# Kernel optimization log

Hardware: AMD Instinct MI355X
Metric: run time of the kernel (lower is better)

The kernel has to match this reference:

```python
import jax, jax.numpy as jnp
import numpy as np

B, C, S, N, V = 8, 16, 512, 512, 128
EPS = 1e-5

def setup_inputs() -> dict:
    key = jax.random.key(0)
    ks = jax.random.split(key, 9)
    def u(k, shape, scale):
        return jax.random.uniform(k, shape, jnp.float32, -scale, scale)
    attn_scale = 12 * np.sqrt(3.0 / (S * N * V))      # custom attn_init for query / key.left / value2
    xav_vs = np.sqrt(6.0 / (V + S))                    # xavier_uniform for (C, V, S) or (C, S, V)
    xav_nv = np.sqrt(6.0 / (N + V))                    # xavier_uniform for (C, N, V)
    return {
        "x": jax.random.normal(ks[0], (B, C, S, N), jnp.float32),
        "wq": u(ks[1], (C, N, V), attn_scale),          # query weight (other_features=S)
        "k_left": u(ks[2], (C, V, S), attn_scale),      # key left (attn_init)
        "k_right": u(ks[3], (C, N, V), xav_nv),         # key right (xavier)
        "v1_left": u(ks[4], (C, V, S), xav_vs),         # value1 left (xavier, attn_init=False)
        "v1_right": u(ks[5], (C, N, V), attn_scale),    # value1 right (attn_init scale)
        "v2_w": u(ks[6], (C, V, S), attn_scale),        # value2 weight (other_features=N)
        "gamma": jnp.ones((C,), jnp.float32),
        "beta": jnp.zeros((C,), jnp.float32),
    }

def batch_scaler(y, gamma, beta):
    # normalize over dims (0, 2, 3); per-channel affine
    mean = jnp.mean(y, axis=(0, 2, 3), keepdims=True)
    var = jnp.mean(jnp.square(y - mean), axis=(0, 2, 3), keepdims=True)
    yhat = (y - mean) * jax.lax.rsqrt(var + EPS)
    return yhat * gamma[None, :, None, None] + beta[None, :, None, None]

def reference(x, wq, k_left, k_right, v1_left, v1_right, v2_w, gamma, beta):
    # x: [B,C,S,N]
    q = jnp.matmul(x, wq)                               # [B,C,S,V]
    k = jnp.matmul(jnp.matmul(k_left, x), k_right)       # (C,V,S)@x -> [B,C,V,N] @ (C,N,V) -> [B,C,V,V]
    attn = jax.nn.softmax(jnp.einsum('bcsv,bcwv->bcsw', q, k), axis=-1)  # q @ k^T, softmax last dim
    v1 = jnp.matmul(jnp.matmul(v1_left, x), v1_right)    # [B,C,V,V]
    v2 = jnp.matmul(v2_w, x)                             # [B,C,V,N]
    v = jnp.matmul(v1, v2)                               # [B,C,V,N]
    y = x + jnp.matmul(attn, v)                          # [B,C,S,N]
    return batch_scaler(y, gamma, beta)
```

## Files before the change

kernel.cpp:

```cpp
#include <hip/hip_runtime.h>
#include <math.h>


typedef short  bf16x8 __attribute__((ext_vector_type(8)));
typedef short  short8 __attribute__((ext_vector_type(8)));
typedef float  f32x4  __attribute__((ext_vector_type(4)));

__device__ __forceinline__ unsigned short f2bf(float f) {
    union { float f; unsigned u; } v; v.f = f;
    return (unsigned short)((v.u + 0x7FFF + ((v.u >> 16) & 1)) >> 16);
}
__device__ __forceinline__ float bf2f(unsigned short u) {
    union { unsigned u; float f; } v; v.u = (unsigned)u << 16; return v.f;
}

__device__ __forceinline__ void gload16(const void* g, void* l)
{
    __builtin_amdgcn_global_load_lds(
        (const __attribute__((address_space(1))) void*)g,
        (__attribute__((address_space(3))) void*)l, 16, 0, 0);
}

constexpr size_t OB_XB   = 0;
constexpr size_t OB_XT   = OB_XB  + 67108864;
constexpr size_t OB_KLB  = OB_XT  + 67108864;
constexpr size_t OB_V1LB = OB_KLB + 2097152;
constexpr size_t OB_V2WB = OB_V1LB+ 2097152;
constexpr size_t OB_WQT  = OB_V2WB+ 2097152;
constexpr size_t OB_KRT  = OB_WQT + 2097152;
constexpr size_t OB_V1RT = OB_KRT + 2097152;
constexpr size_t OB_BUF  = OB_V1RT+ 2097152;
constexpr size_t OB_V2T  = OB_BUF + 33554432;
constexpr size_t OB_KM   = OB_V2T + 16777216;
constexpr size_t OB_V1M  = OB_KM  + 4194304;
constexpr size_t OB_ATT  = OB_V1M + 4194304;
constexpr size_t OB_VT   = OB_ATT + 16777216;
constexpr size_t OB_ST   = OB_VT  + 16777216;

template<int NSTEPS, int MF, int NF>
__device__ __forceinline__ void mmcore(const char* __restrict__ Ab, int ldaB,
                                       const char* __restrict__ Bb, int ldbB,
                                       f32x4 (&acc)[MF][NF],
                                       char* __restrict__ smA, char* __restrict__ smB,
                                       int wm, int wn)
{
    const int tid = threadIdx.x;
    const int w = tid >> 6, l = tid & 63, g = l >> 4, lr = l & 15;
    const int rl = l >> 3, ch = l & 7;

#pragma unroll 1
    for (int t = 0; t < NSTEPS; ++t) {
#pragma unroll
        for (int j = 0; j < 4; ++j) {
            const int row = w * 32 + j * 8 + rl;
            gload16(Ab + (size_t)row * ldaB + t * 128 + ((ch ^ (row & 7)) * 16),
                    smA + (w * 32 + j * 8) * 128);
        }
#pragma unroll
        for (int j = 0; j < 4; ++j) {
            const int row = w * 32 + j * 8 + rl;
            gload16(Bb + (size_t)row * ldbB + t * 128 + ((ch ^ (row & 7)) * 16),
                    smB + (w * 32 + j * 8) * 128);
        }
        __syncthreads();
#pragma unroll
        for (int ks = 0; ks < 2; ++ks) {
            bf16x8 av[MF], bv[NF];
            const int cc = ks * 4 + g;
#pragma unroll
            for (int i = 0; i < MF; ++i) { int rw = wm + i * 16 + lr;
                av[i] = *(const bf16x8*)(smA + rw * 128 + ((cc ^ (rw & 7)) * 16)); }
#pragma unroll
            for (int j = 0; j < NF; ++j) { int rw = wn + j * 16 + lr;
                bv[j] = *(const bf16x8*)(smB + rw * 128 + ((cc ^ (rw & 7)) * 16)); }
#pragma unroll
            for (int i = 0; i < MF; ++i)
#pragma unroll
                for (int j = 0; j < NF; ++j)
                    acc[i][j] = __builtin_amdgcn_mfma_f32_16x16x32_bf16(av[i], bv[j], acc[i][j], 0, 0, 0);
        }
        __syncthreads();
    }
}

__device__ __forceinline__ void epi_write_rm(const f32x4 (&acc)[4][4], char* sm)
{
    const int tid = threadIdx.x, w = tid >> 6, l = tid & 63, g = l >> 4, lr = l & 15;
    const int wm = (w >> 1) * 64, wn = (w & 1) * 64;
#pragma unroll
    for (int i = 0; i < 4; ++i)
#pragma unroll
        for (int j = 0; j < 4; ++j) {
            const int row = wm + i * 16 + g * 4, col = wn + j * 16 + lr;
#pragma unroll
            for (int r = 0; r < 4; ++r)
                *(unsigned short*)(sm + (row + r) * 272 + col * 2) = f2bf(acc[i][j][r]);
        }
}

__device__ __forceinline__ void epi_write_tr(const f32x4 (&acc)[4][4], char* sm)
{
    const int tid = threadIdx.x, w = tid >> 6, l = tid & 63, g = l >> 4, lr = l & 15;
    const int wm = (w >> 1) * 64, wn = (w & 1) * 64;
#pragma unroll
    for (int i = 0; i < 4; ++i)
#pragma unroll
        for (int j = 0; j < 4; ++j) {
            const int rv = wm + i * 16 + g * 4, cn = wn + j * 16 + lr;
            ushort4 pk = make_ushort4(f2bf(acc[i][j][0]), f2bf(acc[i][j][1]),
                                      f2bf(acc[i][j][2]), f2bf(acc[i][j][3]));
            *(ushort4*)(sm + cn * 272 + rv * 2) = pk;
        }
}

__device__ __forceinline__ void epi_flush(const char* sm, unsigned short* gout, int ldg)
{
    const int tid = threadIdx.x;
    const int r0 = tid >> 4, q = tid & 15;
#pragma unroll
    for (int rep = 0; rep < 8; ++rep) {
        const int row = rep * 16 + r0;
        *(short8*)((short*)gout + (size_t)row * ldg + q * 8) =
            *(const short8*)(sm + row * 272 + q * 16);
    }
    __syncthreads();
}

__global__ __launch_bounds__(256) void k_prep(const float* __restrict__ kl,
                                              const float* __restrict__ v1l,
                                              const float* __restrict__ v2w,
                                              const float* __restrict__ wq,
                                              const float* __restrict__ kr,
                                              const float* __restrict__ v1r,
                                              unsigned short* __restrict__ klb,
                                              unsigned short* __restrict__ v1lb,
                                              unsigned short* __restrict__ v2wb,
                                              unsigned short* __restrict__ wqt,
                                              unsigned short* __restrict__ krt,
                                              unsigned short* __restrict__ v1rt,
                                              float* __restrict__ stats)
{
    __shared__ float tl[64][65];
    const int id = blockIdx.x, tid = threadIdx.x;
    if (id == 0 && tid < 64) stats[tid] = 0.f;
    if (id < 192) {
        const int sel = id >> 6, blk = id & 63;
        const float* src = sel == 0 ? kl : sel == 1 ? v1l : v2w;
        unsigned short* dst = sel == 0 ? klb : sel == 1 ? v1lb : v2wb;
#pragma unroll
        for (int r = 0; r < 4; ++r) {
            const int i = blk * 1024 + r * 256 + tid;
            float4 v = ((const float4*)src)[i];
            ((ushort4*)dst)[i] = make_ushort4(f2bf(v.x), f2bf(v.y), f2bf(v.z), f2bf(v.w));
        }
        return;
    }
    const int id2 = id - 192;
    const int p = id2 >> 4, rem = id2 & 15, by = rem >> 1, bx = rem & 1;
    const int widx = p >> 4, c = p & 15;
    const float* s = (widx == 0 ? wq : widx == 1 ? kr : v1r) + (size_t)c * 65536;
    unsigned short* d = (widx == 0 ? wqt : widx == 1 ? krt : v1rt) + (size_t)c * 65536;
    const int r0 = by * 64, c0 = bx * 64;
    const int rr = tid >> 4, cc = (tid & 15) * 4;
#pragma unroll
    for (int rep = 0; rep < 4; ++rep) {
        int row = rep * 16 + rr;
        float4 v = *(const float4*)(s + (size_t)(r0 + row) * 128 + c0 + cc);
        tl[cc + 0][row] = v.x; tl[cc + 1][row] = v.y; tl[cc + 2][row] = v.z; tl[cc + 3][row] = v.w;
    }
    __syncthreads();
#pragma unroll
    for (int rep = 0; rep < 4; ++rep) {
        int crow = rep * 16 + rr;
        *(ushort4*)(d + (size_t)(c0 + crow) * 512 + r0 + cc) =
            make_ushort4(f2bf(tl[crow][cc]), f2bf(tl[crow][cc + 1]),
                         f2bf(tl[crow][cc + 2]), f2bf(tl[crow][cc + 3]));
    }
}

__global__ __launch_bounds__(256, 2) void k_wx(const unsigned short* __restrict__ klb,
                                               const unsigned short* __restrict__ v1lb,
                                               const unsigned short* __restrict__ v2wb,
                                               const float* __restrict__ x,
                                               unsigned short* __restrict__ bufb,
                                               unsigned short* __restrict__ v2t)
{
    __shared__ char smem[34816];
    char* smA = smem;
    char* smX = smem + 16384;
    const int mt = blockIdx.x >> 2, n0 = blockIdx.x & 3, bc = blockIdx.y, c = bc & 15;
    const unsigned short* W = mt == 0 ? klb : mt == 1 ? v1lb : v2wb;
    const char* Wb = (const char*)(W + (size_t)c * 65536);
    const float* xs = x + (size_t)bc * 262144 + n0 * 128;
    const int tid = threadIdx.x, w = tid >> 6, l = tid & 63, g = l >> 4, lr = l & 15;
    const int rl = l >> 3, ch = l & 7;
    const int wm = (w >> 1) * 64, wn = (w & 1) * 64;
    const int nq = (tid & 31) * 4, sp2 = (tid >> 5) * 2;

    f32x4 acc[4][4] = {};
    float4 fr[8];
#pragma unroll
    for (int k = 0; k < 4; ++k) {
        const int sl = k * 16 + sp2;
        fr[k * 2 + 0] = *(const float4*)(xs + (size_t)(sl) * 512 + nq);
        fr[k * 2 + 1] = *(const float4*)(xs + (size_t)(sl + 1) * 512 + nq);
    }

#pragma unroll 1
    for (int t = 0; t < 8; ++t) {
#pragma unroll
        for (int j = 0; j < 4; ++j) {
            const int row = w * 32 + j * 8 + rl;
            gload16(Wb + (size_t)row * 1024 + t * 128 + ((ch ^ (row & 7)) * 16),
                    smA + (w * 32 + j * 8) * 128);
        }
#pragma unroll
        for (int k = 0; k < 4; ++k) {
            const int sl = k * 16 + sp2;
            const float4 f0 = fr[k * 2 + 0];
            const float4 f1 = fr[k * 2 + 1];
            const unsigned p0 = f2bf(f0.x) | ((unsigned)f2bf(f1.x) << 16);
            const unsigned p1 = f2bf(f0.y) | ((unsigned)f2bf(f1.y) << 16);
            const unsigned p2 = f2bf(f0.z) | ((unsigned)f2bf(f1.z) << 16);
            const unsigned p3 = f2bf(f0.w) | ((unsigned)f2bf(f1.w) << 16);
            const int cl = sl >> 3, bic = (sl * 2) & 15;
#pragma unroll
            for (int i = 0; i < 4; ++i) {
                const int n = nq + i;
                const unsigned v = (i == 0) ? p0 : (i == 1) ? p1 : (i == 2) ? p2 : p3;
                *(unsigned*)(smX + n * 136 + ((cl ^ (n & 7)) << 4) + bic) = v;
            }
        }
        __syncthreads();
        if (t < 7) {
#pragma unroll
            for (int k = 0; k < 4; ++k) {
                const int sl = k * 16 + sp2;
                fr[k * 2 + 0] = *(const float4*)(xs + (size_t)((t + 1) * 64 + sl) * 512 + nq);
                fr[k * 2 + 1] = *(const float4*)(xs + (size_t)((t + 1) * 64 + sl + 1) * 512 + nq);
            }
        }
#pragma unroll
        for (int ks = 0; ks < 2; ++ks) {
            const int cc = ks * 4 + g;
            bf16x8 av[4], bv[4];
#pragma unroll
            for (int i = 0; i < 4; ++i) { const int rw = wm + i * 16 + lr;
                av[i] = *(const bf16x8*)(smA + rw * 128 + ((cc ^ (rw & 7)) * 16)); }
#pragma unroll
            for (int j = 0; j < 4; ++j) {
                const int n = wn + j * 16 + lr;
                const char* p = smX + n * 136 + ((cc ^ (n & 7)) << 4);
                union { unsigned long long u[2]; bf16x8 v; } tmp;
                tmp.u[0] = *(const unsigned long long*)(p);
                tmp.u[1] = *(const unsigned long long*)(p + 8);
                bv[j] = tmp.v;
            }
#pragma unroll
            for (int i = 0; i < 4; ++i)
#pragma unroll
                for (int j = 0; j < 4; ++j)
                    acc[i][j] = __builtin_amdgcn_mfma_f32_16x16x32_bf16(av[i], bv[j], acc[i][j], 0, 0, 0);
        }
        __syncthreads();
    }

    if (mt < 2) {
        epi_write_rm(acc, smem);
        __syncthreads();
        epi_flush(smem, bufb + (size_t)bc * 131072 + (size_t)mt * 65536 + n0 * 128, 512);
    } else {
        epi_write_tr(acc, smem);
        __syncthreads();
        epi_flush(smem, v2t + (size_t)bc * 65536 + (size_t)n0 * 16384, 128);
    }
}

__global__ __launch_bounds__(256, 2) void k_kr(const unsigned short* __restrict__ bufb,
                                               const unsigned short* __restrict__ krt,
                                               const unsigned short* __restrict__ v1rt,
                                               unsigned short* __restrict__ kmat,
                                               unsigned short* __restrict__ v1m)
{
    __shared__ char smem[34816];
    char* smA = smem; char* smB = smem + 16384;
    const int mt = blockIdx.x, bc = blockIdx.y, c = bc & 15;
    const int w = threadIdx.x >> 6;
    f32x4 acc[4][4] = {};
    mmcore<8, 4, 4>((const char*)(bufb + (size_t)bc * 131072 + (size_t)mt * 65536), 1024,
                    (const char*)((mt ? v1rt : krt) + (size_t)c * 65536), 1024, acc, smA, smB,
                    (w >> 1) * 64, (w & 1) * 64);
    epi_write_rm(acc, smem);
    __syncthreads();
    epi_flush(smem, (mt ? v1m : kmat) + (size_t)bc * 16384, 128);
}

__global__ __launch_bounds__(256, 2) void k_qat(const float* __restrict__ x,
                                                const unsigned short* __restrict__ wqt,
                                                const unsigned short* __restrict__ kmat,
                                                unsigned short* __restrict__ attn)
{
    __shared__ char smem[49152];
    char* smA  = smem;
    char* smB  = smem + 16384;
    char* qlds = smem;
    char* smB2 = smem + 32768;
    const int mt = blockIdx.x, bc = blockIdx.y, c = bc & 15;
    const int tid = threadIdx.x, w = tid >> 6, l = tid & 63, g = l >> 4, lr = l & 15;
    const int rl = l >> 3, ch = l & 7;
    const int wm = (w >> 1) * 64, wn = (w & 1) * 64;

    f32x4 acc[4][4] = {};
    {
        const float* Ax = x + (size_t)bc * 262144 + (size_t)(mt * 128) * 512;
        const char* Bw = (const char*)(wqt + (size_t)c * 65536);
        const int ar = tid >> 4, fq = tid & 15;
#pragma unroll 1
        for (int t = 0; t < 8; ++t) {
#pragma unroll
            for (int j = 0; j < 4; ++j) {
                const int row = w * 32 + j * 8 + rl;
                gload16(Bw + (size_t)row * 1024 + t * 128 + ((ch ^ (row & 7)) * 16),
                        smB + (w * 32 + j * 8) * 128);
            }
            float4 frq[8];
#pragma unroll
            for (int it = 0; it < 8; ++it) {
                const int row = it * 16 + ar;
                frq[it] = *(const float4*)(Ax + (size_t)row * 512 + t * 64 + fq * 4);
            }
#pragma unroll
            for (int it = 0; it < 8; ++it) {
                const int row = it * 16 + ar;
                ushort4 o = make_ushort4(f2bf(frq[it].x), f2bf(frq[it].y),
                                         f2bf(frq[it].z), f2bf(frq[it].w));
                *(ushort4*)(smA + row * 128 + (((fq >> 1) ^ (row & 7)) * 16) + (fq & 1) * 8) = o;
            }
            __syncthreads();
#pragma unroll
            for (int ks = 0; ks < 2; ++ks) {
                const int cc2 = ks * 4 + g;
                bf16x8 av[4], bv[4];
#pragma unroll
                for (int i = 0; i < 4; ++i) { const int rw = wm + i * 16 + lr;
                    av[i] = *(const bf16x8*)(smA + rw * 128 + ((cc2 ^ (rw & 7)) * 16)); }
#pragma unroll
                for (int j = 0; j < 4; ++j) { const int rw = wn + j * 16 + lr;
                    bv[j] = *(const bf16x8*)(smB + rw * 128 + ((cc2 ^ (rw & 7)) * 16)); }
#pragma unroll
                for (int i = 0; i < 4; ++i)
#pragma unroll
                    for (int j = 0; j < 4; ++j)
                        acc[i][j] = __builtin_amdgcn_mfma_f32_16x16x32_bf16(av[i], bv[j], acc[i][j], 0, 0, 0);
            }
            __syncthreads();
        }
    }
    {
        const int t = wn >> 6;
#pragma unroll
        for (int i = 0; i < 4; ++i)
#pragma unroll
            for (int j = 0; j < 4; ++j) {
                const int k6 = j * 16 + lr;
                const int chunk = k6 >> 3, eb = (k6 & 7) << 1;
#pragma unroll
                for (int r = 0; r < 4; ++r) {
                    const int row = wm + i * 16 + g * 4 + r;
                    *(unsigned short*)(qlds + t * 16384 + row * 128 +
                                       ((chunk ^ (row & 7)) << 4) + eb) = f2bf(acc[i][j][r]);
                }
            }
    }
    __syncthreads();

    f32x4 acc2[2][8] = {};
    const char* Kb = (const char*)(kmat + (size_t)bc * 16384);
#pragma unroll
    for (int t = 0; t < 2; ++t) {
#pragma unroll
        for (int j = 0; j < 4; ++j) {
            const int row = w * 32 + j * 8 + rl;
            gload16(Kb + (size_t)row * 256 + t * 128 + ((ch ^ (row & 7)) * 16),
                    smB2 + (w * 32 + j * 8) * 128);
        }
        __syncthreads();
#pragma unroll
        for (int ks = 0; ks < 2; ++ks) {
            const int cc2 = ks * 4 + g;
            bf16x8 av[2], bv[8];
#pragma unroll
            for (int i = 0; i < 2; ++i) { const int rw = w * 32 + i * 16 + lr;
                av[i] = *(const bf16x8*)(qlds + t * 16384 + rw * 128 + ((cc2 ^ (rw & 7)) * 16)); }
#pragma unroll
            for (int j = 0; j < 8; ++j) { const int rw = j * 16 + lr;
                bv[j] = *(const bf16x8*)(smB2 + rw * 128 + ((cc2 ^ (rw & 7)) * 16)); }
#pragma unroll
            for (int i = 0; i < 2; ++i)
#pragma unroll
                for (int j = 0; j < 8; ++j)
                    acc2[i][j] = __builtin_amdgcn_mfma_f32_16x16x32_bf16(av[i], bv[j], acc2[i][j], 0, 0, 0);
        }
        __syncthreads();
    }

    char* wsl = smem + w * 8704;
    unsigned short* ob = attn + (size_t)bc * 65536 + (size_t)(mt * 128 + w * 32) * 128;
#pragma unroll
    for (int i = 0; i < 2; ++i)
#pragma unroll
        for (int r = 0; r < 4; ++r) {
            float mx = -3e38f;
#pragma unroll
            for (int fj = 0; fj < 8; ++fj) mx = fmaxf(mx, acc2[i][fj][r]);
#pragma unroll
            for (int d = 1; d < 16; d <<= 1) mx = fmaxf(mx, __shfl_xor(mx, d));
            float s = 0.f, e[8];
#pragma unroll
            for (int fj = 0; fj < 8; ++fj) { e[fj] = __expf(acc2[i][fj][r] - mx); s += e[fj]; }
#pragma unroll
            for (int d = 1; d < 16; d <<= 1) s += __shfl_xor(s, d);
            const float inv = 1.f / s;
            const int rowh = i * 16 + g * 4 + r;
#pragma unroll
            for (int fj = 0; fj < 8; ++fj)
                *(unsigned short*)(wsl + rowh * 272 + (fj * 16 + lr) * 2) = f2bf(e[fj] * inv);
        }
#pragma unroll
    for (int rep = 0; rep < 8; ++rep) {
        const int row = rep * 4 + (l >> 4);
        *(short8*)((short*)ob + (size_t)row * 128 + (l & 15) * 8) =
            *(const short8*)(wsl + row * 272 + (l & 15) * 16);
    }
}

__global__ __launch_bounds__(256, 2) void k_v(const unsigned short* __restrict__ v2t,
                                              const unsigned short* __restrict__ v1m,
                                              unsigned short* __restrict__ vt)
{
    __shared__ char smem[34816];
    char* smA = smem; char* smB = smem + 16384;
    const int mt = blockIdx.x, bc = blockIdx.y;
    const int w = threadIdx.x >> 6;
    f32x4 acc[4][4] = {};
    mmcore<2, 4, 4>((const char*)(v2t + (size_t)bc * 65536 + (size_t)mt * 16384), 256,
                    (const char*)(v1m + (size_t)bc * 16384), 256, acc, smA, smB,
                    (w >> 1) * 64, (w & 1) * 64);
    epi_write_rm(acc, smem);
    __syncthreads();
    epi_flush(smem, vt + (size_t)bc * 65536 + (size_t)mt * 16384, 128);
}

__global__ __launch_bounds__(256, 2) void k_y(const unsigned short* __restrict__ attn,
                                              const unsigned short* __restrict__ vt,
                                              const float* __restrict__ x,
                                              unsigned short* __restrict__ yb,
                                              float* __restrict__ stats)
{
    __shared__ char smem[34816];
    __shared__ float r1[4], r2[4];
    char* smA = smem; char* smB = smem + 16384;
    const int nx = blockIdx.x, my = blockIdx.y, bc = blockIdx.z, c = bc & 15;
    const int tid = threadIdx.x, w = tid >> 6, l = tid & 63, g = l >> 4, lr = l & 15;
    f32x4 acc[4][4] = {};
    mmcore<2, 4, 4>((const char*)(attn + (size_t)bc * 65536 + (size_t)my * 16384), 256,
                    (const char*)(vt + (size_t)bc * 65536 + (size_t)nx * 16384), 256, acc, smA, smB,
                    (w >> 1) * 64, (w & 1) * 64);
    const float* xw = x + (size_t)bc * 262144 + (size_t)my * 128 * 512 + nx * 128;
    const int wm = (w >> 1) * 64, wn = (w & 1) * 64;
    float lsum = 0.f, lss = 0.f;
#pragma unroll
    for (int i = 0; i < 4; ++i)
#pragma unroll
        for (int j = 0; j < 4; ++j)
#pragma unroll
            for (int r = 0; r < 4; ++r) {
                const int row = wm + i * 16 + g * 4 + r, col = wn + j * 16 + lr;
                const float yv = acc[i][j][r] + xw[(size_t)row * 512 + col];
                lsum += yv; lss += yv * yv;
                *(unsigned short*)(smem + row * 272 + col * 2) = f2bf(yv);
            }
#pragma unroll
    for (int d = 32; d >= 1; d >>= 1) { lsum += __shfl_xor(lsum, d); lss += __shfl_xor(lss, d); }
    if (l == 0) { r1[w] = lsum; r2[w] = lss; }
    __syncthreads();
    epi_flush(smem, yb + (size_t)bc * 262144 + (size_t)my * 128 * 512 + nx * 128, 512);
    if (tid == 0) {
        atomicAdd(&stats[c * 2 + 0], r1[0] + r1[1] + r1[2] + r1[3]);
        atomicAdd(&stats[c * 2 + 1], r2[0] + r2[1] + r2[2] + r2[3]);
    }
}

__global__ __launch_bounds__(256) void k_norm(const unsigned short* __restrict__ yb,
                                              float* __restrict__ out,
                                              const float* __restrict__ stats,
                                              const float* __restrict__ gamma,
                                              const float* __restrict__ beta)
{
    __shared__ float ssc[16], ssh[16];
    if (threadIdx.x < 16) {
        const int c = threadIdx.x;
        const float cnt  = 2097152.f;
        const float mean = stats[c * 2 + 0] / cnt;
        const float var  = stats[c * 2 + 1] / cnt - mean * mean;
        const float sc   = rsqrtf(var + 1e-5f) * gamma[c];
        ssc[c] = sc;
        ssh[c] = beta[c] - mean * sc;
    }
    __syncthreads();
    const int tot = 4194304;
    for (int i = blockIdx.x * 256 + threadIdx.x; i < tot; i += gridDim.x * 256) {
        const long e = (long)i * 8;
        const int c = (int)(e >> 18) & 15;
        const float sc = ssc[c];
        const float sh = ssh[c];
        short8 v = ((const short8*)yb)[i];
        float4 o0, o1;
        o0.x = bf2f((unsigned short)v[0]) * sc + sh;
        o0.y = bf2f((unsigned short)v[1]) * sc + sh;
        o0.z = bf2f((unsigned short)v[2]) * sc + sh;
        o0.w = bf2f((unsigned short)v[3]) * sc + sh;
        o1.x = bf2f((unsigned short)v[4]) * sc + sh;
        o1.y = bf2f((unsigned short)v[5]) * sc + sh;
        o1.z = bf2f((unsigned short)v[6]) * sc + sh;
        o1.w = bf2f((unsigned short)v[7]) * sc + sh;
        ((float4*)out)[(size_t)i * 2 + 0] = o0;
        ((float4*)out)[(size_t)i * 2 + 1] = o1;
    }
}

extern "C" void kernel_launch(void* const* d_in, const int* in_sizes, int n_in,
                              void* d_out, int out_size, void* d_ws, size_t ws_size,
                              hipStream_t stream)
{
    (void)in_sizes; (void)n_in; (void)out_size; (void)ws_size;
    const float* x     = (const float*)d_in[0];
    const float* wq    = (const float*)d_in[1];
    const float* kl    = (const float*)d_in[2];
    const float* kr    = (const float*)d_in[3];
    const float* v1l   = (const float*)d_in[4];
    const float* v1r   = (const float*)d_in[5];
    const float* v2w   = (const float*)d_in[6];
    const float* gamma = (const float*)d_in[7];
    const float* beta  = (const float*)d_in[8];
    float* out = (float*)d_out;
    char*  ws  = (char*)d_ws;

    unsigned short* yb   = (unsigned short*)(ws + OB_XB);
    unsigned short* klb  = (unsigned short*)(ws + OB_KLB);
    unsigned short* v1lb = (unsigned short*)(ws + OB_V1LB);
    unsigned short* v2wb = (unsigned short*)(ws + OB_V2WB);
    unsigned short* wqt  = (unsigned short*)(ws + OB_WQT);
    unsigned short* krt  = (unsigned short*)(ws + OB_KRT);
    unsigned short* v1rt = (unsigned short*)(ws + OB_V1RT);
    unsigned short* bufb = (unsigned short*)(ws + OB_BUF);
    unsigned short* v2t  = (unsigned short*)(ws + OB_V2T);
    unsigned short* kmat = (unsigned short*)(ws + OB_KM);
    unsigned short* v1m  = (unsigned short*)(ws + OB_V1M);
    unsigned short* attn = (unsigned short*)(ws + OB_ATT);
    unsigned short* vt   = (unsigned short*)(ws + OB_VT);
    float*          st   = (float*)(ws + OB_ST);

    hipLaunchKernelGGL(k_prep,  dim3(960),       dim3(256), 0, stream,
                       kl, v1l, v2w, wq, kr, v1r, klb, v1lb, v2wb, wqt, krt, v1rt, st);
    hipLaunchKernelGGL(k_wx,    dim3(12, 128),   dim3(256), 0, stream, klb, v1lb, v2wb, x, bufb, v2t);
    hipLaunchKernelGGL(k_kr,    dim3(2, 128),    dim3(256), 0, stream, bufb, krt, v1rt, kmat, v1m);
    hipLaunchKernelGGL(k_qat,   dim3(4, 128),    dim3(256), 0, stream, x, wqt, kmat, attn);
    hipLaunchKernelGGL(k_v,     dim3(4, 128),    dim3(256), 0, stream, v2t, v1m, vt);
    hipLaunchKernelGGL(k_y,     dim3(4, 4, 128), dim3(256), 0, stream, attn, vt, x, yb, st);
    hipLaunchKernelGGL(k_norm,  dim3(2048),      dim3(256), 0, stream, yb, out, st, gamma, beta);
}
```

Baseline: 232.7 us.

## Merge the three weight-times-x GEMMs into one block per column tile

k_wx now launches one block per (n0, bc) instead of one per weight matrix. Each block computes the k_left and v1_left products together in one pass over x, sharing the bf16-converted x tile in LDS across two accumulator sets, then runs a second pass for the v2 weight. This cuts the x conversion and staging work from three passes to two per tile. In exchange it uses more LDS and registers per block (two accumulator sets) and launches a third as many blocks, which lowers occupancy and parallelism.

```diff
diff --git a/kernel.cpp b/kernel.cpp
--- a/kernel.cpp
+++ b/kernel.cpp
@@ -185,19 +185,20 @@
                                                unsigned short* __restrict__ bufb,
                                                unsigned short* __restrict__ v2t)
 {
-    __shared__ char smem[34816];
-    char* smA = smem;
-    char* smX = smem + 16384;
-    const int mt = blockIdx.x >> 2, n0 = blockIdx.x & 3, bc = blockIdx.y, c = bc & 15;
-    const unsigned short* W = mt == 0 ? klb : mt == 1 ? v1lb : v2wb;
-    const char* Wb = (const char*)(W + (size_t)c * 65536);
+    __shared__ char smem[50176];
+    char* smA0 = smem;
+    char* smA1 = smem + 16384;
+    char* smX  = smem + 32768;
+    const int n0 = blockIdx.x, bc = blockIdx.y, c = bc & 15;
+    const char* Wb0 = (const char*)(klb  + (size_t)c * 65536);
+    const char* Wb1 = (const char*)(v1lb + (size_t)c * 65536);
+    const char* Wb2 = (const char*)(v2wb + (size_t)c * 65536);
     const float* xs = x + (size_t)bc * 262144 + n0 * 128;
     const int tid = threadIdx.x, w = tid >> 6, l = tid & 63, g = l >> 4, lr = l & 15;
     const int rl = l >> 3, ch = l & 7;
     const int wm = (w >> 1) * 64, wn = (w & 1) * 64;
     const int nq = (tid & 31) * 4, sp2 = (tid >> 5) * 2;
 
-    f32x4 acc[4][4] = {};
     float4 fr[8];
 #pragma unroll
     for (int k = 0; k < 4; ++k) {
@@ -206,13 +207,20 @@
         fr[k * 2 + 1] = *(const float4*)(xs + (size_t)(sl + 1) * 512 + nq);
     }
 
+    f32x4 acc0[4][4] = {}, acc1[4][4] = {};
 #pragma unroll 1
     for (int t = 0; t < 8; ++t) {
 #pragma unroll
         for (int j = 0; j < 4; ++j) {
             const int row = w * 32 + j * 8 + rl;
-            gload16(Wb + (size_t)row * 1024 + t * 128 + ((ch ^ (row & 7)) * 16),
-                    smA + (w * 32 + j * 8) * 128);
+            gload16(Wb0 + (size_t)row * 1024 + t * 128 + ((ch ^ (row & 7)) * 16),
+                    smA0 + (w * 32 + j * 8) * 128);
+        }
+#pragma unroll
+        for (int j = 0; j < 4; ++j) {
+            const int row = w * 32 + j * 8 + rl;
+            gload16(Wb1 + (size_t)row * 1024 + t * 128 + ((ch ^ (row & 7)) * 16),
+                    smA1 + (w * 32 + j * 8) * 128);
         }
 #pragma unroll
         for (int k = 0; k < 4; ++k) {
@@ -245,9 +253,6 @@
             const int cc = ks * 4 + g;
             bf16x8 av[4], bv[4];
 #pragma unroll
-            for (int i = 0; i < 4; ++i) { const int rw = wm + i * 16 + lr;
-                av[i] = *(const bf16x8*)(smA + rw * 128 + ((cc ^ (rw & 7)) * 16)); }
-#pragma unroll
             for (int j = 0; j < 4; ++j) {
                 const int n = wn + j * 16 + lr;
                 const char* p = smX + n * 136 + ((cc ^ (n & 7)) << 4);
@@ -257,23 +262,99 @@
                 bv[j] = tmp.v;
             }
 #pragma unroll
+            for (int i = 0; i < 4; ++i) { const int rw = wm + i * 16 + lr;
+                av[i] = *(const bf16x8*)(smA0 + rw * 128 + ((cc ^ (rw & 7)) * 16)); }
+#pragma unroll
             for (int i = 0; i < 4; ++i)
 #pragma unroll
                 for (int j = 0; j < 4; ++j)
-                    acc[i][j] = __builtin_amdgcn_mfma_f32_16x16x32_bf16(av[i], bv[j], acc[i][j], 0, 0, 0);
-        }
-        __syncthreads();
-    }
-
-    if (mt < 2) {
-        epi_write_rm(acc, smem);
-        __syncthreads();
-        epi_flush(smem, bufb + (size_t)bc * 131072 + (size_t)mt * 65536 + n0 * 128, 512);
-    } else {
-        epi_write_tr(acc, smem);
-        __syncthreads();
-        epi_flush(smem, v2t + (size_t)bc * 65536 + (size_t)n0 * 16384, 128);
-    }
+                    acc0[i][j] = __builtin_amdgcn_mfma_f32_16x16x32_bf16(av[i], bv[j], acc0[i][j], 0, 0, 0);
+#pragma unroll
+            for (int i = 0; i < 4; ++i) { const int rw = wm + i * 16 + lr;
+                av[i] = *(const bf16x8*)(smA1 + rw * 128 + ((cc ^ (rw & 7)) * 16)); }
+#pragma unroll
+            for (int i = 0; i < 4; ++i)
+#pragma unroll
+                for (int j = 0; j < 4; ++j)
+                    acc1[i][j] = __builtin_amdgcn_mfma_f32_16x16x32_bf16(av[i], bv[j], acc1[i][j], 0, 0, 0);
+        }
+        __syncthreads();
+    }
+    epi_write_rm(acc0, smem);
+    __syncthreads();
+    epi_flush(smem, bufb + (size_t)bc * 131072 + n0 * 128, 512);
+    epi_write_rm(acc1, smem);
+    __syncthreads();
+    epi_flush(smem, bufb + (size_t)bc * 131072 + 65536 + n0 * 128, 512);
+
+    f32x4 acc2[4][4] = {};
+#pragma unroll
+    for (int k = 0; k < 4; ++k) {
+        const int sl = k * 16 + sp2;
+        fr[k * 2 + 0] = *(const float4*)(xs + (size_t)(sl) * 512 + nq);
+        fr[k * 2 + 1] = *(const float4*)(xs + (size_t)(sl + 1) * 512 + nq);
+    }
+#pragma unroll 1
+    for (int t = 0; t < 8; ++t) {
+#pragma unroll
+        for (int j = 0; j < 4; ++j) {
+            const int row = w * 32 + j * 8 + rl;
+            gload16(Wb2 + (size_t)row * 1024 + t * 128 + ((ch ^ (row & 7)) * 16),
+                    smA0 + (w * 32 + j * 8) * 128);
+        }
+#pragma unroll
+        for (int k = 0; k < 4; ++k) {
+            const int sl = k * 16 + sp2;
+            const float4 f0 = fr[k * 2 + 0];
+            const float4 f1 = fr[k * 2 + 1];
+            const unsigned p0 = f2bf(f0.x) | ((unsigned)f2bf(f1.x) << 16);
+            const unsigned p1 = f2bf(f0.y) | ((unsigned)f2bf(f1.y) << 16);
+            const unsigned p2 = f2bf(f0.z) | ((unsigned)f2bf(f1.z) << 16);
+            const unsigned p3 = f2bf(f0.w) | ((unsigned)f2bf(f1.w) << 16);
+            const int cl = sl >> 3, bic = (sl * 2) & 15;
+#pragma unroll
+            for (int i = 0; i < 4; ++i) {
+                const int n = nq + i;
+                const unsigned v = (i == 0) ? p0 : (i == 1) ? p1 : (i == 2) ? p2 : p3;
+                *(unsigned*)(smX + n * 136 + ((cl ^ (n & 7)) << 4) + bic) = v;
+            }
+        }
+        __syncthreads();
+        if (t < 7) {
+#pragma unroll
+            for (int k = 0; k < 4; ++k) {
+                const int sl = k * 16 + sp2;
+                fr[k * 2 + 0] = *(const float4*)(xs + (size_t)((t + 1) * 64 + sl) * 512 + nq);
+                fr[k * 2 + 1] = *(const float4*)(xs + (size_t)((t + 1) * 64 + sl + 1) * 512 + nq);
+            }
+        }
+#pragma unroll
+        for (int ks = 0; ks < 2; ++ks) {
+            const int cc = ks * 4 + g;
+            bf16x8 av[4], bv[4];
+#pragma unroll
+            for (int i = 0; i < 4; ++i) { const int rw = wm + i * 16 + lr;
+                av[i] = *(const bf16x8*)(smA0 + rw * 128 + ((cc ^ (rw & 7)) * 16)); }
+#pragma unroll
+            for (int j = 0; j < 4; ++j) {
+                const int n = wn + j * 16 + lr;
+                const char* p = smX + n * 136 + ((cc ^ (n & 7)) << 4);
+                union { unsigned long long u[2]; bf16x8 v; } tmp;
+                tmp.u[0] = *(const unsigned long long*)(p);
+                tmp.u[1] = *(const unsigned long long*)(p + 8);
+                bv[j] = tmp.v;
+            }
+#pragma unroll
+            for (int i = 0; i < 4; ++i)
+#pragma unroll
+                for (int j = 0; j < 4; ++j)
+                    acc2[i][j] = __builtin_amdgcn_mfma_f32_16x16x32_bf16(av[i], bv[j], acc2[i][j], 0, 0, 0);
+        }
+        __syncthreads();
+    }
+    epi_write_tr(acc2, smem);
+    __syncthreads();
+    epi_flush(smem, v2t + (size_t)bc * 65536 + (size_t)n0 * 16384, 128);
 }
 
 __global__ __launch_bounds__(256, 2) void k_kr(const unsigned short* __restrict__ bufb,
@@ -563,7 +644,7 @@
 
     hipLaunchKernelGGL(k_prep,  dim3(960),       dim3(256), 0, stream,
                        kl, v1l, v2w, wq, kr, v1r, klb, v1lb, v2wb, wqt, krt, v1rt, st);
-    hipLaunchKernelGGL(k_wx,    dim3(12, 128),   dim3(256), 0, stream, klb, v1lb, v2wb, x, bufb, v2t);
+    hipLaunchKernelGGL(k_wx,    dim3(4, 128),    dim3(256), 0, stream, klb, v1lb, v2wb, x, bufb, v2t);
     hipLaunchKernelGGL(k_kr,    dim3(2, 128),    dim3(256), 0, stream, bufb, krt, v1rt, kmat, v1m);
     hipLaunchKernelGGL(k_qat,   dim3(4, 128),    dim3(256), 0, stream, x, wqt, kmat, attn);
     hipLaunchKernelGGL(k_v,     dim3(4, 128),    dim3(256), 0, stream, v2t, v1m, vt);
```

Result: no change. 230.7 us (-0.8%).

## Fuse three weight-by-x GEMMs into one block sharing the converted x tile

Applied to the files above, without the earlier changes.

k_wx now computes the key-left, value1-left and value2 products in a single block per (n0, bc), so each x tile is loaded and converted to bf16 once instead of three times. The grid shrinks from 12x128 to 4x128 blocks. Each block now holds three 4x4 accumulator sets, uses 64KB of LDS, and drops the register prefetch of the next x tile. The x LDS layout also changes to an unpadded 128-byte row stride with a different XOR swizzle and single 16-byte reads. In exchange, register pressure rises, occupancy falls, and there are fewer blocks to fill the GPU, with no prefetch left to hide x load latency.

```diff
diff --git a/kernel.cpp b/kernel.cpp
--- a/kernel.cpp
+++ b/kernel.cpp
@@ -185,95 +185,97 @@
                                                unsigned short* __restrict__ bufb,
                                                unsigned short* __restrict__ v2t)
 {
-    __shared__ char smem[34816];
-    char* smA = smem;
-    char* smX = smem + 16384;
-    const int mt = blockIdx.x >> 2, n0 = blockIdx.x & 3, bc = blockIdx.y, c = bc & 15;
-    const unsigned short* W = mt == 0 ? klb : mt == 1 ? v1lb : v2wb;
-    const char* Wb = (const char*)(W + (size_t)c * 65536);
+    __shared__ char smem[65536];
+    char* smA0 = smem;
+    char* smA1 = smem + 16384;
+    char* smA2 = smem + 32768;
+    char* smX  = smem + 49152;
+    const int n0 = blockIdx.x, bc = blockIdx.y, c = bc & 15;
+    const char* Wb0 = (const char*)(klb  + (size_t)c * 65536);
+    const char* Wb1 = (const char*)(v1lb + (size_t)c * 65536);
+    const char* Wb2 = (const char*)(v2wb + (size_t)c * 65536);
     const float* xs = x + (size_t)bc * 262144 + n0 * 128;
     const int tid = threadIdx.x, w = tid >> 6, l = tid & 63, g = l >> 4, lr = l & 15;
     const int rl = l >> 3, ch = l & 7;
     const int wm = (w >> 1) * 64, wn = (w & 1) * 64;
     const int nq = (tid & 31) * 4, sp2 = (tid >> 5) * 2;
 
-    f32x4 acc[4][4] = {};
-    float4 fr[8];
-#pragma unroll
-    for (int k = 0; k < 4; ++k) {
-        const int sl = k * 16 + sp2;
-        fr[k * 2 + 0] = *(const float4*)(xs + (size_t)(sl) * 512 + nq);
-        fr[k * 2 + 1] = *(const float4*)(xs + (size_t)(sl + 1) * 512 + nq);
-    }
+    f32x4 acc0[4][4] = {}, acc1[4][4] = {}, acc2[4][4] = {};
 
 #pragma unroll 1
     for (int t = 0; t < 8; ++t) {
 #pragma unroll
         for (int j = 0; j < 4; ++j) {
             const int row = w * 32 + j * 8 + rl;
-            gload16(Wb + (size_t)row * 1024 + t * 128 + ((ch ^ (row & 7)) * 16),
-                    smA + (w * 32 + j * 8) * 128);
+            const size_t off = (size_t)row * 1024 + t * 128 + ((ch ^ (row & 7)) * 16);
+            gload16(Wb0 + off, smA0 + (w * 32 + j * 8) * 128);
+            gload16(Wb1 + off, smA1 + (w * 32 + j * 8) * 128);
+            gload16(Wb2 + off, smA2 + (w * 32 + j * 8) * 128);
         }
 #pragma unroll
         for (int k = 0; k < 4; ++k) {
             const int sl = k * 16 + sp2;
-            const float4 f0 = fr[k * 2 + 0];
-            const float4 f1 = fr[k * 2 + 1];
+            const float4 f0 = *(const float4*)(xs + (size_t)(t * 64 + sl) * 512 + nq);
+            const float4 f1 = *(const float4*)(xs + (size_t)(t * 64 + sl + 1) * 512 + nq);
             const unsigned p0 = f2bf(f0.x) | ((unsigned)f2bf(f1.x) << 16);
             const unsigned p1 = f2bf(f0.y) | ((unsigned)f2bf(f1.y) << 16);
             const unsigned p2 = f2bf(f0.z) | ((unsigned)f2bf(f1.z) << 16);
             const unsigned p3 = f2bf(f0.w) | ((unsigned)f2bf(f1.w) << 16);
-            const int cl = sl >> 3, bic = (sl * 2) & 15;
+            const int cl = sl >> 3, bic = (sl & 7) * 2;
 #pragma unroll
             for (int i = 0; i < 4; ++i) {
                 const int n = nq + i;
                 const unsigned v = (i == 0) ? p0 : (i == 1) ? p1 : (i == 2) ? p2 : p3;
-                *(unsigned*)(smX + n * 136 + ((cl ^ (n & 7)) << 4) + bic) = v;
+                *(unsigned*)(smX + n * 128 + ((cl ^ ((n >> 2) & 7)) << 4) + bic) = v;
             }
         }
         __syncthreads();
-        if (t < 7) {
-#pragma unroll
-            for (int k = 0; k < 4; ++k) {
-                const int sl = k * 16 + sp2;
-                fr[k * 2 + 0] = *(const float4*)(xs + (size_t)((t + 1) * 64 + sl) * 512 + nq);
-                fr[k * 2 + 1] = *(const float4*)(xs + (size_t)((t + 1) * 64 + sl + 1) * 512 + nq);
-            }
-        }
 #pragma unroll
         for (int ks = 0; ks < 2; ++ks) {
             const int cc = ks * 4 + g;
-            bf16x8 av[4], bv[4];
-#pragma unroll
-            for (int i = 0; i < 4; ++i) { const int rw = wm + i * 16 + lr;
-                av[i] = *(const bf16x8*)(smA + rw * 128 + ((cc ^ (rw & 7)) * 16)); }
+            bf16x8 bv[4], av[4];
 #pragma unroll
             for (int j = 0; j < 4; ++j) {
                 const int n = wn + j * 16 + lr;
-                const char* p = smX + n * 136 + ((cc ^ (n & 7)) << 4);
-                union { unsigned long long u[2]; bf16x8 v; } tmp;
-                tmp.u[0] = *(const unsigned long long*)(p);
-                tmp.u[1] = *(const unsigned long long*)(p + 8);
-                bv[j] = tmp.v;
-            }
+                bv[j] = *(const bf16x8*)(smX + n * 128 + ((cc ^ ((n >> 2) & 7)) << 4));
+            }
+#pragma unroll
+            for (int i = 0; i < 4; ++i) { const int rw = wm + i * 16 + lr;
+                av[i] = *(const bf16x8*)(smA0 + rw * 128 + ((cc ^ (rw & 7)) * 16)); }
 #pragma unroll
             for (int i = 0; i < 4; ++i)
 #pragma unroll
                 for (int j = 0; j < 4; ++j)
-                    acc[i][j] = __builtin_amdgcn_mfma_f32_16x16x32_bf16(av[i], bv[j], acc[i][j], 0, 0, 0);
+                    acc0[i][j] = __builtin_amdgcn_mfma_f32_16x16x32_bf16(av[i], bv[j], acc0[i][j], 0, 0, 0);
+#pragma unroll
+            for (int i = 0; i < 4; ++i) { const int rw = wm + i * 16 + lr;
+                av[i] = *(const bf16x8*)(smA1 + rw * 128 + ((cc ^ (rw & 7)) * 16)); }
+#pragma unroll
+            for (int i = 0; i < 4; ++i)
+#pragma unroll
+                for (int j = 0; j < 4; ++j)
+                    acc1[i][j] = __builtin_amdgcn_mfma_f32_16x16x32_bf16(av[i], bv[j], acc1[i][j], 0, 0, 0);
+#pragma unroll
+            for (int i = 0; i < 4; ++i) { const int rw = wm + i * 16 + lr;
+                av[i] = *(const bf16x8*)(smA2 + rw * 128 + ((cc ^ (rw & 7)) * 16)); }
+#pragma unroll
+            for (int i = 0; i < 4; ++i)
+#pragma unroll
+                for (int j = 0; j < 4; ++j)
+                    acc2[i][j] = __builtin_amdgcn_mfma_f32_16x16x32_bf16(av[i], bv[j], acc2[i][j], 0, 0, 0);
         }
         __syncthreads();
     }
 
-    if (mt < 2) {
-        epi_write_rm(acc, smem);
-        __syncthreads();
-        epi_flush(smem, bufb + (size_t)bc * 131072 + (size_t)mt * 65536 + n0 * 128, 512);
-    } else {
-        epi_write_tr(acc, smem);
-        __syncthreads();
-        epi_flush(smem, v2t + (size_t)bc * 65536 + (size_t)n0 * 16384, 128);
-    }
+    epi_write_rm(acc0, smem);
+    __syncthreads();
+    epi_flush(smem, bufb + (size_t)bc * 131072 + n0 * 128, 512);
+    epi_write_rm(acc1, smem);
+    __syncthreads();
+    epi_flush(smem, bufb + (size_t)bc * 131072 + 65536 + n0 * 128, 512);
+    epi_write_tr(acc2, smem);
+    __syncthreads();
+    epi_flush(smem, v2t + (size_t)bc * 65536 + (size_t)n0 * 16384, 128);
 }
 
 __global__ __launch_bounds__(256, 2) void k_kr(const unsigned short* __restrict__ bufb,
@@ -563,7 +565,7 @@
 
     hipLaunchKernelGGL(k_prep,  dim3(960),       dim3(256), 0, stream,
                        kl, v1l, v2w, wq, kr, v1r, klb, v1lb, v2wb, wqt, krt, v1rt, st);
-    hipLaunchKernelGGL(k_wx,    dim3(12, 128),   dim3(256), 0, stream, klb, v1lb, v2wb, x, bufb, v2t);
+    hipLaunchKernelGGL(k_wx,    dim3(4, 128),    dim3(256), 0, stream, klb, v1lb, v2wb, x, bufb, v2t);
     hipLaunchKernelGGL(k_kr,    dim3(2, 128),    dim3(256), 0, stream, bufb, krt, v1rt, kmat, v1m);
     hipLaunchKernelGGL(k_qat,   dim3(4, 128),    dim3(256), 0, stream, x, wqt, kmat, attn);
     hipLaunchKernelGGL(k_v,     dim3(4, 128),    dim3(256), 0, stream, v2t, v1m, vt);
```

After: 243.7 us. +4.8%, slower.
